# Performance work log

Hardware: AMD Instinct MI355X
Metric: run time of the kernel (lower is better)

The kernel has to match this reference:

```python
import jax, jax.numpy as jnp
import numpy as np

B, L = 64, 8192
WIN = 3            # unfold window size
H = 90             # surrogate MLP hidden width (brains-py default)
N_ELEC = 7         # total electrodes; data on 2,3,4; controls on 0,1,5,6
AMP = 28.5         # electrode_effects amplification


def setup_inputs() -> dict:
    key = jax.random.key(0)
    ks = jax.random.split(key, 16)
    x = jax.random.normal(ks[0], (B, L), dtype=jnp.float32)
    # 4 learned control voltages (electrodes 0,1,5,6), plausible voltage range
    cv = jax.random.uniform(ks[1], (4,), dtype=jnp.float32, minval=-1.2, maxval=0.6)
    def lin(k, fan_in, fan_out):
        w = jax.random.normal(k, (fan_in, fan_out), dtype=jnp.float32) * np.sqrt(2.0 / fan_in).astype(np.float32)
        return w
    W1 = lin(ks[2], N_ELEC, H); b1 = jnp.zeros((H,), jnp.float32)
    W2 = lin(ks[3], H, H);      b2 = jnp.zeros((H,), jnp.float32)
    W3 = lin(ks[4], H, H);      b3 = jnp.zeros((H,), jnp.float32)
    W4 = lin(ks[5], H, H);      b4 = jnp.zeros((H,), jnp.float32)
    W5 = lin(ks[6], H, H);      b5 = jnp.zeros((H,), jnp.float32)
    W6 = lin(ks[7], H, 1);      b6 = jnp.zeros((1,), jnp.float32)
    return {"x": x, "cv": cv,
            "W1": W1, "b1": b1, "W2": W2, "b2": b2, "W3": W3, "b3": b3,
            "W4": W4, "b4": b4, "W5": W5, "b5": b5, "W6": W6, "b6": b6}


def reference(x, cv, W1, b1, W2, b2, W3, b3, W4, b4, W5, b5, W6, b6):
    Bq, Lq = x.shape
    n_win = Lq - WIN + 1
    # sliding windows (unfold(1, 3, 1)): [B, n_win, 3]
    idx = jnp.arange(n_win)[:, None] + jnp.arange(WIN)[None, :]
    win = x[:, idx]  # [B, n_win, 3]
    # assemble 7-electrode input: cv[0:2] | data window | cv[2:4]
    cv_lo = jnp.broadcast_to(cv[:2], (Bq, n_win, 2))
    cv_hi = jnp.broadcast_to(cv[2:], (Bq, n_win, 2))
    z = jnp.concatenate([cv_lo, win, cv_hi], axis=-1)  # [B, n_win, 7]
    h = jax.nn.relu(z @ W1 + b1)
    h = jax.nn.relu(h @ W2 + b2)
    h = jax.nn.relu(h @ W3 + b3)
    h = jax.nn.relu(h @ W4 + b4)
    h = jax.nn.relu(h @ W5 + b5)
    out = (h @ W6 + b6) * AMP  # [B, n_win, 1]
    return out[..., 0]  # squeeze -> [B, n_win]
```

## Files before the change

### kernel.cpp

```cpp
#include <hip/hip_runtime.h>

#define NB   64
#define LSEQ 8192
#define NW   8190
#define HD   90
#define AMPF 28.5f

typedef _Float16 half8  __attribute__((ext_vector_type(8)));
typedef float    f32x4  __attribute__((ext_vector_type(4)));
typedef __fp16   fp16x2 __attribute__((ext_vector_type(2)));

union FragU { uint4 u; half8 h; };

__device__ __forceinline__ unsigned pk2(float a, float b) {
  fp16x2 v = __builtin_amdgcn_cvt_pkrtz(a, b);
  return __builtin_bit_cast(unsigned, v);
}
__device__ __forceinline__ unsigned pkmax0(unsigned w) {
  unsigned r;
  asm("v_pk_max_f16 %0, %1, %2" : "=v"(r) : "v"(w), "v"(0u));
  return r;
}
__device__ __forceinline__ int imin(int a, int b) { return a < b ? a : b; }

__global__ void dnpu_pack(const float* __restrict__ W1, const float* __restrict__ b1,
                          const float* __restrict__ W2, const float* __restrict__ b2,
                          const float* __restrict__ W3, const float* __restrict__ b3,
                          const float* __restrict__ W4, const float* __restrict__ b4,
                          const float* __restrict__ W5, const float* __restrict__ b5,
                          const float* __restrict__ W6, const float* __restrict__ b6,
                          uint4* __restrict__ frags) {
  int tid = blockIdx.x * blockDim.x + threadIdx.x;
  if (tid >= 81 * 64) return;
  int f = tid >> 6, lane = tid & 63;
  int nl = lane & 15, g = lane >> 4;
  FragU u;
  if (f < 6) {
    int n = 16 * f + nl;
#pragma unroll
    for (int i = 0; i < 8; ++i) {
      float val = 0.f;
      if (g == 0) {
        if (n < HD) { if (i < 7) val = W1[i * HD + n]; else val = b1[n]; }
        else if (n == HD && i == 7) val = 1.0f;
      }
      u.h[i] = (_Float16)val;
    }
  } else if (f < 78) {
    int q = f - 6, L = q / 18, r = q % 18, t2 = r / 3, s = r % 3;
    const float* W    = (L == 0) ? W2 : (L == 1) ? W3 : (L == 2) ? W4 : W5;
    const float* bias = (L == 0) ? b2 : (L == 1) ? b3 : (L == 2) ? b4 : b5;
    int n = 16 * t2 + nl;
#pragma unroll
    for (int i = 0; i < 8; ++i) {
      int k = 32 * s + ((i >> 2) << 4) + (g << 2) + (i & 3);
      float val = 0.f;
      if (n < HD)      { if (k < HD) val = W[k * HD + n]; else if (k == HD) val = bias[n]; }
      else if (n == HD && k == HD) val = 1.0f;
      u.h[i] = (_Float16)val;
    }
  } else {
    int s = f - 78;
    int n = nl;
#pragma unroll
    for (int i = 0; i < 8; ++i) {
      int k = 32 * s + ((i >> 2) << 4) + (g << 2) + (i & 3);
      float val = 0.f;
      if (n == 0) { if (k < HD) val = W6[k]; else if (k == HD) val = b6[0]; }
      u.h[i] = (_Float16)val;
    }
  }
  frags[f * 64 + lane] = u.u;
}

__device__ __forceinline__ void hidden(const uint4* __restrict__ wfr, int lane,
                                       uint4 (&B)[2][3], const f32x4& zz) {
  unsigned P[2][6][2];
#pragma unroll
  for (int t2 = 0; t2 < 6; ++t2) {
    FragU Wf[3];
#pragma unroll
    for (int s = 0; s < 3; ++s) Wf[s].u = wfr[(t2 * 3 + s) * 64 + lane];
#pragma unroll
    for (int t = 0; t < 2; ++t) {
      f32x4 a = __builtin_amdgcn_mfma_f32_16x16x32_f16(
                  Wf[0].h, __builtin_bit_cast(half8, B[t][0]), zz, 0, 0, 0);
      a = __builtin_amdgcn_mfma_f32_16x16x32_f16(
                  Wf[1].h, __builtin_bit_cast(half8, B[t][1]), a, 0, 0, 0);
      a = __builtin_amdgcn_mfma_f32_16x16x32_f16(
                  Wf[2].h, __builtin_bit_cast(half8, B[t][2]), a, 0, 0, 0);
      P[t][t2][0] = pkmax0(pk2(a[0], a[1]));
      P[t][t2][1] = pkmax0(pk2(a[2], a[3]));
    }
  }
#pragma unroll
  for (int t = 0; t < 2; ++t)
#pragma unroll
    for (int s = 0; s < 3; ++s)
      B[t][s] = make_uint4(P[t][2 * s][0], P[t][2 * s][1],
                           P[t][2 * s + 1][0], P[t][2 * s + 1][1]);
}

__global__ __launch_bounds__(256, 2)
void dnpu_mfma(const float* __restrict__ x, const float* __restrict__ cv,
               const uint4* __restrict__ frags, float* __restrict__ out) {
  __shared__ uint4 wfr[18 * 64];
  const int tid  = threadIdx.x;
  const int lane = tid & 63, wid = tid >> 6;
  const int g = lane >> 4, nl = lane & 15;
  const int b = blockIdx.y;

  f32x4 zz = (f32x4)(0.f);
  asm volatile("" : "+v"(zz));

  for (int i = tid; i < 18 * 64; i += 256) wfr[i] = frags[6 * 64 + i];

  const float c0 = cv[0], c1 = cv[1], c2 = cv[2], c3 = cv[3];
  const float* xr = x + (size_t)b * LSEQ;
  const int rowbase = blockIdx.x * 128 + wid * 32;

  uint4 B[2][3];

  {
    FragU A1[6];
#pragma unroll
    for (int t2 = 0; t2 < 6; ++t2) A1[t2].u = frags[t2 * 64 + lane];
    unsigned P[2][6][2];
#pragma unroll
    for (int t = 0; t < 2; ++t) {
      const int w  = rowbase + t * 16 + nl;
      const int xi = imin(w, LSEQ - 3);
      const float x0 = xr[xi], x1 = xr[xi + 1], x2 = xr[xi + 2];
      half8 B1;
#pragma unroll
      for (int i = 0; i < 8; ++i) B1[i] = (_Float16)0.f;
      if (g == 0) {
        B1[0] = (_Float16)c0; B1[1] = (_Float16)c1;
        B1[2] = (_Float16)x0; B1[3] = (_Float16)x1; B1[4] = (_Float16)x2;
        B1[5] = (_Float16)c2; B1[6] = (_Float16)c3; B1[7] = (_Float16)1.0f;
      }
#pragma unroll
      for (int t2 = 0; t2 < 6; ++t2) {
        f32x4 a = __builtin_amdgcn_mfma_f32_16x16x32_f16(A1[t2].h, B1, zz, 0, 0, 0);
        P[t][t2][0] = pkmax0(pk2(a[0], a[1]));
        P[t][t2][1] = pkmax0(pk2(a[2], a[3]));
      }
    }
#pragma unroll
    for (int t = 0; t < 2; ++t)
#pragma unroll
      for (int s = 0; s < 3; ++s)
        B[t][s] = make_uint4(P[t][2 * s][0], P[t][2 * s][1],
                             P[t][2 * s + 1][0], P[t][2 * s + 1][1]);
  }

  __syncthreads();
  hidden(wfr, lane, B, zz);
  __syncthreads();
  for (int i = tid; i < 18 * 64; i += 256) wfr[i] = frags[(6 + 18) * 64 + i];
  __syncthreads();
  hidden(wfr, lane, B, zz);
  __syncthreads();
  for (int i = tid; i < 18 * 64; i += 256) wfr[i] = frags[(6 + 36) * 64 + i];
  __syncthreads();
  hidden(wfr, lane, B, zz);
  __syncthreads();
  for (int i = tid; i < 18 * 64; i += 256) wfr[i] = frags[(6 + 54) * 64 + i];
  __syncthreads();
  hidden(wfr, lane, B, zz);

  {
    FragU A6[3];
#pragma unroll
    for (int s = 0; s < 3; ++s) A6[s].u = frags[(78 + s) * 64 + lane];
#pragma unroll
    for (int t = 0; t < 2; ++t) {
      f32x4 a = __builtin_amdgcn_mfma_f32_16x16x32_f16(
                  A6[0].h, __builtin_bit_cast(half8, B[t][0]), zz, 0, 0, 0);
      a = __builtin_amdgcn_mfma_f32_16x16x32_f16(
                  A6[1].h, __builtin_bit_cast(half8, B[t][1]), a, 0, 0, 0);
      a = __builtin_amdgcn_mfma_f32_16x16x32_f16(
                  A6[2].h, __builtin_bit_cast(half8, B[t][2]), a, 0, 0, 0);
      if (g == 0) {
        const int row = rowbase + t * 16 + nl;
        if (row < NW) out[(size_t)b * NW + row] = a[0] * AMPF;
      }
    }
  }
}

extern "C" void kernel_launch(void* const* d_in, const int* in_sizes, int n_in,
                              void* d_out, int out_size, void* d_ws, size_t ws_size,
                              hipStream_t stream) {
  const float* x  = (const float*)d_in[0];
  const float* cv = (const float*)d_in[1];
  const float* W1 = (const float*)d_in[2];
  const float* b1 = (const float*)d_in[3];
  const float* W2 = (const float*)d_in[4];
  const float* b2 = (const float*)d_in[5];
  const float* W3 = (const float*)d_in[6];
  const float* b3 = (const float*)d_in[7];
  const float* W4 = (const float*)d_in[8];
  const float* b4 = (const float*)d_in[9];
  const float* W5 = (const float*)d_in[10];
  const float* b5 = (const float*)d_in[11];
  const float* W6 = (const float*)d_in[12];
  const float* b6 = (const float*)d_in[13];
  float* out = (float*)d_out;
  uint4* frags = (uint4*)d_ws;

  hipLaunchKernelGGL(dnpu_pack, dim3(21), dim3(256), 0, stream,
                     W1, b1, W2, b2, W3, b3, W4, b4, W5, b5, W6, b6, frags);
  hipLaunchKernelGGL(dnpu_mfma, dim3(64, NB), dim3(256), 0, stream,
                     x, cv, frags, out);
}
```

Baseline: 47.59 us.

## Switch MLP layers from 16x16x32 to 32x32x16 MFMA tiles

Each wave now computes its 32 windows as a single 32-column tile using 32x32x16 f16 MFMA instead of two 16-column tiles with 16x16x32. The pack kernel re-lays out the weight fragments to match the new K/N layout, and the first-layer input fragment is packed directly as half2 pairs. The aim is fewer MFMA and pack instructions and fewer weight-fragment reuse issues per layer. The trade-offs are larger accumulators (16 floats) and wasted MFMA work in the K=8 first layer and the single-output last layer, both of which now use 32x32 tiles.

New measurement: 49.85 us. 1.05x slower.

```diff
diff --git a/kernel.cpp b/kernel.cpp
--- a/kernel.cpp
+++ b/kernel.cpp
@@ -7,7 +7,7 @@
 #define AMPF 28.5f
 
 typedef _Float16 half8  __attribute__((ext_vector_type(8)));
-typedef float    f32x4  __attribute__((ext_vector_type(4)));
+typedef float    f32x16 __attribute__((ext_vector_type(16)));
 typedef __fp16   fp16x2 __attribute__((ext_vector_type(2)));
 
 union FragU { uint4 u; half8 h; };
@@ -33,38 +33,37 @@
   int tid = blockIdx.x * blockDim.x + threadIdx.x;
   if (tid >= 81 * 64) return;
   int f = tid >> 6, lane = tid & 63;
-  int nl = lane & 15, g = lane >> 4;
+  int c = lane & 31, g = lane >> 5;
   FragU u;
-  if (f < 6) {
-    int n = 16 * f + nl;
+  if (f < 3) {
+    int n = 32 * f + c;
 #pragma unroll
     for (int i = 0; i < 8; ++i) {
+      int k = 4 * g + (i & 3) + 8 * (i >> 2);
       float val = 0.f;
-      if (g == 0) {
-        if (n < HD) { if (i < 7) val = W1[i * HD + n]; else val = b1[n]; }
-        else if (n == HD && i == 7) val = 1.0f;
-      }
+      if (n < HD)      { if (k < 7) val = W1[k * HD + n]; else if (k == 7) val = b1[n]; }
+      else if (n == HD && k == 7) val = 1.0f;
       u.h[i] = (_Float16)val;
     }
-  } else if (f < 78) {
-    int q = f - 6, L = q / 18, r = q % 18, t2 = r / 3, s = r % 3;
+  } else if (f < 75) {
+    int q = f - 3, L = q / 18, r = q % 18, t2 = r / 6, s = r % 6;
     const float* W    = (L == 0) ? W2 : (L == 1) ? W3 : (L == 2) ? W4 : W5;
     const float* bias = (L == 0) ? b2 : (L == 1) ? b3 : (L == 2) ? b4 : b5;
-    int n = 16 * t2 + nl;
+    int n = 32 * t2 + c;
 #pragma unroll
     for (int i = 0; i < 8; ++i) {
-      int k = 32 * s + ((i >> 2) << 4) + (g << 2) + (i & 3);
+      int k = 16 * s + 4 * g + (i & 3) + 8 * (i >> 2);
       float val = 0.f;
       if (n < HD)      { if (k < HD) val = W[k * HD + n]; else if (k == HD) val = bias[n]; }
       else if (n == HD && k == HD) val = 1.0f;
       u.h[i] = (_Float16)val;
     }
   } else {
-    int s = f - 78;
-    int n = nl;
+    int s = f - 75;
+    int n = c;
 #pragma unroll
     for (int i = 0; i < 8; ++i) {
-      int k = 32 * s + ((i >> 2) << 4) + (g << 2) + (i & 3);
+      int k = 16 * s + 4 * g + (i & 3) + 8 * (i >> 2);
       float val = 0.f;
       if (n == 0) { if (k < HD) val = W6[k]; else if (k == HD) val = b6[0]; }
       u.h[i] = (_Float16)val;
@@ -73,32 +72,31 @@
   frags[f * 64 + lane] = u.u;
 }
 
+__device__ __forceinline__ void pack_t2(const f32x16& a, uint4& b0, uint4& b1) {
+  b0 = make_uint4(pkmax0(pk2(a[0],  a[1])),  pkmax0(pk2(a[2],  a[3])),
+                  pkmax0(pk2(a[4],  a[5])),  pkmax0(pk2(a[6],  a[7])));
+  b1 = make_uint4(pkmax0(pk2(a[8],  a[9])),  pkmax0(pk2(a[10], a[11])),
+                  pkmax0(pk2(a[12], a[13])), pkmax0(pk2(a[14], a[15])));
+}
+
 __device__ __forceinline__ void hidden(const uint4* __restrict__ wfr, int lane,
-                                       uint4 (&B)[2][3], const f32x4& zz) {
-  unsigned P[2][6][2];
+                                       uint4 (&B)[6], const f32x16& zz) {
+  uint4 Bn[6];
 #pragma unroll
-  for (int t2 = 0; t2 < 6; ++t2) {
-    FragU Wf[3];
+  for (int t2 = 0; t2 < 3; ++t2) {
+    FragU Af0; Af0.u = wfr[(t2 * 6 + 0) * 64 + lane];
+    f32x16 a = __builtin_amdgcn_mfma_f32_32x32x16_f16(
+                 Af0.h, __builtin_bit_cast(half8, B[0]), zz, 0, 0, 0);
 #pragma unroll
-    for (int s = 0; s < 3; ++s) Wf[s].u = wfr[(t2 * 3 + s) * 64 + lane];
-#pragma unroll
-    for (int t = 0; t < 2; ++t) {
-      f32x4 a = __builtin_amdgcn_mfma_f32_16x16x32_f16(
-                  Wf[0].h, __builtin_bit_cast(half8, B[t][0]), zz, 0, 0, 0);
-      a = __builtin_amdgcn_mfma_f32_16x16x32_f16(
-                  Wf[1].h, __builtin_bit_cast(half8, B[t][1]), a, 0, 0, 0);
-      a = __builtin_amdgcn_mfma_f32_16x16x32_f16(
-                  Wf[2].h, __builtin_bit_cast(half8, B[t][2]), a, 0, 0, 0);
-      P[t][t2][0] = pkmax0(pk2(a[0], a[1]));
-      P[t][t2][1] = pkmax0(pk2(a[2], a[3]));
+    for (int s = 1; s < 6; ++s) {
+      FragU Af; Af.u = wfr[(t2 * 6 + s) * 64 + lane];
+      a = __builtin_amdgcn_mfma_f32_32x32x16_f16(
+            Af.h, __builtin_bit_cast(half8, B[s]), a, 0, 0, 0);
     }
+    pack_t2(a, Bn[2 * t2], Bn[2 * t2 + 1]);
   }
 #pragma unroll
-  for (int t = 0; t < 2; ++t)
-#pragma unroll
-    for (int s = 0; s < 3; ++s)
-      B[t][s] = make_uint4(P[t][2 * s][0], P[t][2 * s][1],
-                           P[t][2 * s + 1][0], P[t][2 * s + 1][1]);
+  for (int i = 0; i < 6; ++i) B[i] = Bn[i];
 }
 
 __global__ __launch_bounds__(256, 2)
@@ -107,84 +105,64 @@
   __shared__ uint4 wfr[18 * 64];
   const int tid  = threadIdx.x;
   const int lane = tid & 63, wid = tid >> 6;
-  const int g = lane >> 4, nl = lane & 15;
+  const int g = lane >> 5, c = lane & 31;
   const int b = blockIdx.y;
 
-  f32x4 zz = (f32x4)(0.f);
+  f32x16 zz = (f32x16)(0.f);
   asm volatile("" : "+v"(zz));
 
-  for (int i = tid; i < 18 * 64; i += 256) wfr[i] = frags[6 * 64 + i];
+  for (int i = tid; i < 18 * 64; i += 256) wfr[i] = frags[3 * 64 + i];
 
   const float c0 = cv[0], c1 = cv[1], c2 = cv[2], c3 = cv[3];
   const float* xr = x + (size_t)b * LSEQ;
   const int rowbase = blockIdx.x * 128 + wid * 32;
 
-  uint4 B[2][3];
+  uint4 B[6];
 
   {
-    FragU A1[6];
+    const int w  = rowbase + c;
+    const int xi = imin(w, LSEQ - 3);
+    const float x0 = xr[xi], x1 = xr[xi + 1], x2 = xr[xi + 2];
+    uint4 B1u;
+    if (g == 0) B1u = make_uint4(pk2(c0, c1), pk2(x0, x1), 0u, 0u);
+    else        B1u = make_uint4(pk2(x2, c2), pk2(c3, 1.0f), 0u, 0u);
 #pragma unroll
-    for (int t2 = 0; t2 < 6; ++t2) A1[t2].u = frags[t2 * 64 + lane];
-    unsigned P[2][6][2];
-#pragma unroll
-    for (int t = 0; t < 2; ++t) {
-      const int w  = rowbase + t * 16 + nl;
-      const int xi = imin(w, LSEQ - 3);
-      const float x0 = xr[xi], x1 = xr[xi + 1], x2 = xr[xi + 2];
-      half8 B1;
-#pragma unroll
-      for (int i = 0; i < 8; ++i) B1[i] = (_Float16)0.f;
-      if (g == 0) {
-        B1[0] = (_Float16)c0; B1[1] = (_Float16)c1;
-        B1[2] = (_Float16)x0; B1[3] = (_Float16)x1; B1[4] = (_Float16)x2;
-        B1[5] = (_Float16)c2; B1[6] = (_Float16)c3; B1[7] = (_Float16)1.0f;
-      }
-#pragma unroll
-      for (int t2 = 0; t2 < 6; ++t2) {
-        f32x4 a = __builtin_amdgcn_mfma_f32_16x16x32_f16(A1[t2].h, B1, zz, 0, 0, 0);
-        P[t][t2][0] = pkmax0(pk2(a[0], a[1]));
-        P[t][t2][1] = pkmax0(pk2(a[2], a[3]));
-      }
+    for (int t2 = 0; t2 < 3; ++t2) {
+      FragU Af; Af.u = frags[t2 * 64 + lane];
+      f32x16 a = __builtin_amdgcn_mfma_f32_32x32x16_f16(
+                   Af.h, __builtin_bit_cast(half8, B1u), zz, 0, 0, 0);
+      pack_t2(a, B[2 * t2], B[2 * t2 + 1]);
     }
-#pragma unroll
-    for (int t = 0; t < 2; ++t)
-#pragma unroll
-      for (int s = 0; s < 3; ++s)
-        B[t][s] = make_uint4(P[t][2 * s][0], P[t][2 * s][1],
-                             P[t][2 * s + 1][0], P[t][2 * s + 1][1]);
   }
 
   __syncthreads();
   hidden(wfr, lane, B, zz);
   __syncthreads();
-  for (int i = tid; i < 18 * 64; i += 256) wfr[i] = frags[(6 + 18) * 64 + i];
+  for (int i = tid; i < 18 * 64; i += 256) wfr[i] = frags[(3 + 18) * 64 + i];
   __syncthreads();
   hidden(wfr, lane, B, zz);
   __syncthreads();
-  for (int i = tid; i < 18 * 64; i += 256) wfr[i] = frags[(6 + 36) * 64 + i];
+  for (int i = tid; i < 18 * 64; i += 256) wfr[i] = frags[(3 + 36) * 64 + i];
   __syncthreads();
   hidden(wfr, lane, B, zz);
   __syncthreads();
-  for (int i = tid; i < 18 * 64; i += 256) wfr[i] = frags[(6 + 54) * 64 + i];
+  for (int i = tid; i < 18 * 64; i += 256) wfr[i] = frags[(3 + 54) * 64 + i];
   __syncthreads();
   hidden(wfr, lane, B, zz);
 
   {
-    FragU A6[3];
+    FragU A60; A60.u = frags[75 * 64 + lane];
+    f32x16 a = __builtin_amdgcn_mfma_f32_32x32x16_f16(
+                 A60.h, __builtin_bit_cast(half8, B[0]), zz, 0, 0, 0);
 #pragma unroll
-    for (int s = 0; s < 3; ++s) A6[s].u = frags[(78 + s) * 64 + lane];
-#pragma unroll
-    for (int t = 0; t < 2; ++t) {
-      f32x4 a = __builtin_amdgcn_mfma_f32_16x16x32_f16(
-                  A6[0].h, __builtin_bit_cast(half8, B[t][0]), zz, 0, 0, 0);
-      a = __builtin_amdgcn_mfma_f32_16x16x32_f16(
-                  A6[1].h, __builtin_bit_cast(half8, B[t][1]), a, 0, 0, 0);
-      a = __builtin_amdgcn_mfma_f32_16x16x32_f16(
-                  A6[2].h, __builtin_bit_cast(half8, B[t][2]), a, 0, 0, 0);
-      if (g == 0) {
-        const int row = rowbase + t * 16 + nl;
-        if (row < NW) out[(size_t)b * NW + row] = a[0] * AMPF;
-      }
+    for (int s = 1; s < 6; ++s) {
+      FragU Af; Af.u = frags[(75 + s) * 64 + lane];
+      a = __builtin_amdgcn_mfma_f32_32x32x16_f16(
+            Af.h, __builtin_bit_cast(half8, B[s]), a, 0, 0, 0);
+    }
+    if (g == 0) {
+      const int row = rowbase + c;
+      if (row < NW) out[(size_t)b * NW + row] = a[0] * AMPF;
     }
   }
 }
```
